# Kernel tuning notes

Hardware: AMD Instinct MI355X
Metric: run time of the kernel (lower is better)

## Reference

```python
import jax, jax.numpy as jnp
import numpy as np

B, C, D, L, H = 128, 1000, 300, 40, 100


def setup_inputs() -> dict:
    key = jax.random.key(0)
    ks = jax.random.split(key, 16)
    def rn(i, shape, sc=1.0):
        return (jax.random.normal(ks[i], shape, jnp.float32) * sc).astype(jnp.float32)
    return {
        "utt": rn(0, (B, L, D)),
        "sys_slots": rn(1, (B, D), 0.1),
        "conf_slots": rn(2, (B, D), 0.1),
        "conf_values": rn(3, (B, D), 0.1),
        "y_past_state": jax.random.uniform(ks[4], (B, C), jnp.float32),
        "slot_emb": rn(5, (C, D), 0.1),
        "value_emb": rn(6, (C, D), 0.1),
        "Wc": rn(7, (D, 2 * D), 0.05), "bc": jnp.zeros((D,), jnp.float32),
        "conv_w1": rn(8, (D, D, 1), 0.05), "conv_b1": jnp.zeros((D,), jnp.float32),
        "conv_w2": rn(9, (D, D, 2), 0.05), "conv_b2": jnp.zeros((D,), jnp.float32),
        "conv_w3": rn(10, (D, D, 3), 0.05), "conv_b3": jnp.zeros((D,), jnp.float32),
        "Wd": rn(11, (H, D), 0.05), "bd": jnp.zeros((H,), jnp.float32),
        "Wmr": rn(12, (H, D), 0.05), "bmr": jnp.zeros((H,), jnp.float32),
        "Wmc": rn(13, (H, D), 0.05), "bmc": jnp.zeros((H,), jnp.float32),
        "Wj": rn(14, (1, H), 0.05), "bj": jnp.zeros((1,), jnp.float32),
    }


def _conv_relu_pool(x_ncl, w, b):
    # x_ncl: [B, D, L]; w: [F, D, k] -> relu(conv) then global max-pool over time -> [B, F]
    y = jax.lax.conv_general_dilated(x_ncl, w, (1,), 'VALID',
                                     dimension_numbers=('NCH', 'OIH', 'NCH'))
    y = jax.nn.relu(y + b[None, :, None])
    return jnp.max(y, axis=2)


def _sig_linear(x, W, b):
    # Sequential(Sigmoid, Linear): Linear applied to sigmoid(x)
    return jax.nn.sigmoid(x) @ W.T + b


def reference(utt, sys_slots, conf_slots, conf_values, y_past_state,
              slot_emb, value_emb, Wc, bc,
              conv_w1, conv_b1, conv_w2, conv_b2, conv_w3, conv_b3,
              Wd, bd, Wmr, bmr, Wmc, bmc, Wj, bj):
    # CNN utterance encoder: sum of 3 conv branches (filter widths 1,2,3)
    x = jnp.transpose(utt, (0, 2, 1))  # [B, D, L]
    final_utt = (_conv_relu_pool(x, conv_w1, conv_b1)
                 + _conv_relu_pool(x, conv_w2, conv_b2)
                 + _conv_relu_pool(x, conv_w3, conv_b3))  # [B, D]

    # candidates_transform = sigmoid(Linear(cat(slot_emb, value_emb)))
    cand = jax.nn.sigmoid(jnp.concatenate([slot_emb, value_emb], axis=1) @ Wc.T + bc)  # [C, D]

    # fused version of the per-batch repeat/addcmul loop: [B, C, D]
    contrib = cand[None, :, :] * final_utt[:, None, :]

    y1 = _sig_linear(_sig_linear(contrib, Wd, bd), Wj, bj)  # [B, C, 1]

    # system-act request gate: ([C,D]@[D,B]) @ [B,D] -> [C, D]
    m_r = (slot_emb @ sys_slots.T) @ final_utt
    y2 = _sig_linear(_sig_linear(m_r, Wmr, bmr), Wj, bj)  # [C, 1]

    # system-act confirm gate
    m_c = ((slot_emb @ conf_slots.T) * (value_emb @ conf_values.T)) @ final_utt  # [C, D]
    y3 = _sig_linear(_sig_linear(m_c, Wmc, bmc), Wj, bj)  # [C, 1]

    y_presoftmax = y1 + y2[None, :, :] + y3[None, :, :]  # [B, C, 1]
    combine = 0.5
    return combine * y_presoftmax[..., 0] + (1.0 - combine) * y_past_state  # [B, C]
```

## Files before the change

kernel.cpp:

```cpp
#include <hip/hip_runtime.h>
#include <hip/hip_bf16.h>

#define OFF_Y23     0
#define OFF_BDP     4096
#define OFF_WJP     4544
#define OFF_BCP     4992
#define OFF_BMRP    6272
#define OFF_BMCP    6720
#define OFF_WALLT   7168
#define OFF_PBF     1235968
#define OFF_FUBF    20896768
#define OFF_FUBFT   20978688
#define OFF_CATSV   21060608
#define OFF_WCPK    22371328
#define OFF_CANDBF  22780928
#define OFF_WDFRAG  23436288
#define OFF_WMRFRAG 23507968
#define OFF_WMCFRAG 23579648
#define OFF_SYSB    23651328
#define OFF_CONFSB  23733248
#define OFF_CONFVB  23815168
#define OFF_PRBF    23897088
#define OFF_PCBF    24159232
#define OFF_SMRBF   24421376
#define OFF_SMCBF   25076736
#define OFF_XBF     25732096

typedef short bf16x8_t __attribute__((ext_vector_type(8)));
typedef float f32x4_t  __attribute__((ext_vector_type(4)));

__device__ __forceinline__ float sigmoidf_fast(float x) {
    return __builtin_amdgcn_rcpf(1.0f + __expf(-x));
}
__device__ __forceinline__ unsigned short f2bf(float x) {
    unsigned int u = __float_as_uint(x);
    unsigned int r = (u + 0x7FFFu + ((u >> 16) & 1u)) >> 16;
    return (unsigned short)r;
}
__device__ __forceinline__ float bf2f(unsigned short h) {
    return __uint_as_float(((unsigned int)h) << 16);
}

__device__ __forceinline__ float frag_fetch(const float* __restrict__ W, int i) {
    int entry = i >> 3, e = i & 7;
    int kt = entry / 448;
    int r = entry - kt * 448;
    int ni = r >> 6, lane = r & 63;
    int j = ni * 16 + (lane & 15);
    int k = kt * 32 + (lane >> 4) * 8 + e;
    return (j < 100 && k < 300) ? W[j * 300 + k] : 0.0f;
}

__global__ void pack_kernel(const float* __restrict__ w1, const float* __restrict__ w2,
                            const float* __restrict__ w3, const float* __restrict__ Wc,
                            const float* __restrict__ Wd, const float* __restrict__ Wmr,
                            const float* __restrict__ Wmc, const float* __restrict__ sys,
                            const float* __restrict__ confs, const float* __restrict__ confv,
                            const float* __restrict__ bd, const float* __restrict__ Wj,
                            const float* __restrict__ bmr, const float* __restrict__ bmc,
                            const float* __restrict__ bc, const float* __restrict__ slot,
                            const float* __restrict__ value, const float* __restrict__ utt,
                            unsigned short* __restrict__ WallTbf,
                            unsigned short* __restrict__ WdFrag,
                            unsigned short* __restrict__ WmrFrag,
                            unsigned short* __restrict__ WmcFrag,
                            float* __restrict__ bdPad, float* __restrict__ WjPad,
                            float* __restrict__ bmrPad, float* __restrict__ bmcPad,
                            float* __restrict__ bcPad,
                            unsigned short* __restrict__ sysB,
                            unsigned short* __restrict__ confsB,
                            unsigned short* __restrict__ confvB,
                            unsigned short* __restrict__ catsv,
                            unsigned short* __restrict__ WcPk,
                            unsigned short* __restrict__ Xbf) {
    int idx = blockIdx.x * blockDim.x + threadIdx.x;
    if (idx < 614400) {
        int tap = idx / 102400;
        int rem = idx - tap * 102400;
        int f = rem / 320, k = rem % 320;
        float v = 0.0f;
        if (f < 300 && k < 300) {
            int fd = f * 300 + k;
            if (tap == 0)      v = w1[fd];
            else if (tap == 1) v = w2[fd * 2 + 0];
            else if (tap == 2) v = w2[fd * 2 + 1];
            else               v = w3[fd * 3 + (tap - 3)];
        }
        WallTbf[idx] = f2bf(v);
    } else if (idx < 650240) {
        int i = idx - 614400;
        WdFrag[i] = f2bf(frag_fetch(Wd, i));
    } else if (idx < 686080) {
        int i = idx - 650240;
        WmrFrag[i] = f2bf(frag_fetch(Wmr, i));
    } else if (idx < 721920) {
        int i = idx - 686080;
        WmcFrag[i] = f2bf(frag_fetch(Wmc, i));
    } else if (idx < 722032) {
        int j = idx - 721920; bdPad[j] = (j < 100) ? bd[j] : 0.0f;
    } else if (idx < 722144) {
        int j = idx - 722032; WjPad[j] = (j < 100) ? Wj[j] : 0.0f;
    } else if (idx < 722256) {
        int j = idx - 722144; bmrPad[j] = (j < 100) ? bmr[j] : 0.0f;
    } else if (idx < 722368) {
        int j = idx - 722256; bmcPad[j] = (j < 100) ? bmc[j] : 0.0f;
    } else if (idx < 722688) {
        int j = idx - 722368; bcPad[j] = (j < 300) ? bc[j] : 0.0f;
    } else if (idx < 845568) {
        int i = idx - 722688;
        int m = i / 40960, r = i % 40960;
        int b = r / 320, k = r % 320;
        const float* src = (m == 0) ? sys : ((m == 1) ? confs : confv);
        unsigned short* dst = (m == 0) ? sysB : ((m == 1) ? confsB : confvB);
        dst[r] = f2bf((k < 300) ? src[b * 300 + k] : 0.0f);
    } else if (idx < 1500928) {
        int i = idx - 845568;
        int c = i / 640, k = i % 640;
        float v = 0.0f;
        if (c < 1000) {
            if (k < 300)                   v = slot[c * 300 + k];
            else if (k >= 320 && k < 620)  v = value[c * 300 + (k - 320)];
        }
        catsv[i] = f2bf(v);
    } else if (idx < 1705728) {
        int i = idx - 1500928;
        int f = i / 640, k = i % 640;
        float v = 0.0f;
        if (f < 300) {
            if (k < 300)                   v = Wc[f * 600 + k];
            else if (k >= 320 && k < 620)  v = Wc[f * 600 + 300 + (k - 320)];
        }
        WcPk[i] = f2bf(v);
    } else if (idx < 3344128) {
        int i = idx - 1705728;
        int m = i / 320, k = i % 320;
        Xbf[i] = f2bf((k < 300) ? utt[m * 300 + k] : 0.0f);
    }
}

__global__ __launch_bounds__(256, 4) void early_kernel(
        const unsigned short* __restrict__ Xbf, const unsigned short* __restrict__ WallTbf,
        unsigned short* __restrict__ Pbf,
        const unsigned short* __restrict__ catsv, const unsigned short* __restrict__ WcPk,
        const float* __restrict__ bcPad, unsigned short* __restrict__ candbf,
        const unsigned short* __restrict__ sysB, const unsigned short* __restrict__ confsB,
        const unsigned short* __restrict__ confvB,
        unsigned short* __restrict__ Prbf, unsigned short* __restrict__ Pcbf) {
    __shared__ __attribute__((aligned(16))) char smem[25600];
    const int bid = blockIdx.x;
    const int tid = threadIdx.x;
    const int lane = tid & 63, w = tid >> 6;
    const int ln = lane & 15, lq = lane >> 4;

    if (bid >= 112) {
        short* As = (short*)smem;
        short* Bs = (short*)(smem + 5120);
        const int g = bid - 112;
        const int xcd = g & 7;
        const int idx2 = g >> 3;
        const int m0 = (xcd * 10 + idx2 / 15) * 64;
        const int n0 = (idx2 % 15) * 128;
        const int arow = tid >> 2, aq = tid & 3;
        f32x4_t acc[4][2];
        #pragma unroll
        for (int i = 0; i < 4; i++)
            #pragma unroll
            for (int j = 0; j < 2; j++) acc[i][j] = (f32x4_t){0.f, 0.f, 0.f, 0.f};

        const unsigned short* aSrc  = Xbf + (m0 + arow) * 320 + aq * 8;
        const unsigned short* bSrc0 = WallTbf + (n0 + arow) * 320 + aq * 8;
        const unsigned short* bSrc1 = WallTbf + (n0 + 64 + arow) * 320 + aq * 8;
        uint4 pa  = *(const uint4*)(aSrc);
        uint4 pb0 = *(const uint4*)(bSrc0);
        uint4 pb1 = *(const uint4*)(bSrc1);
        *(uint4*)(&As[arow * 40 + aq * 8]) = pa;
        *(uint4*)(&Bs[arow * 40 + aq * 8]) = pb0;
        *(uint4*)(&Bs[(64 + arow) * 40 + aq * 8]) = pb1;
        __syncthreads();

        #pragma unroll 1
        for (int kt = 0; kt < 10; kt++) {
            if (kt < 9) {
                int kk2 = (kt + 1) * 32;
                pa  = *(const uint4*)(aSrc + kk2);
                pb0 = *(const uint4*)(bSrc0 + kk2);
                pb1 = *(const uint4*)(bSrc1 + kk2);
            }
            bf16x8_t a[4], b[2];
            #pragma unroll
            for (int mi = 0; mi < 4; mi++)
                a[mi] = *(const bf16x8_t*)(&As[(mi * 16 + ln) * 40 + lq * 8]);
            #pragma unroll
            for (int ni = 0; ni < 2; ni++)
                b[ni] = *(const bf16x8_t*)(&Bs[(w * 32 + ni * 16 + ln) * 40 + lq * 8]);
            #pragma unroll
            for (int mi = 0; mi < 4; mi++)
                #pragma unroll
                for (int ni = 0; ni < 2; ni++)
                    acc[mi][ni] = __builtin_amdgcn_mfma_f32_16x16x32_bf16(a[mi], b[ni], acc[mi][ni], 0, 0, 0);
            if (kt < 9) {
                __syncthreads();
                *(uint4*)(&As[arow * 40 + aq * 8]) = pa;
                *(uint4*)(&Bs[arow * 40 + aq * 8]) = pb0;
                *(uint4*)(&Bs[(64 + arow) * 40 + aq * 8]) = pb1;
                __syncthreads();
            }
        }
        #pragma unroll
        for (int mi = 0; mi < 4; mi++) {
            #pragma unroll
            for (int ni = 0; ni < 2; ni++) {
                int col = n0 + w * 32 + ni * 16 + ln;
                #pragma unroll
                for (int reg = 0; reg < 4; reg++) {
                    int row = m0 + mi * 16 + lq * 4 + reg;
                    Pbf[row * 1920 + col] = f2bf(acc[mi][ni][reg]);
                }
            }
        }
    } else if (bid < 80) {
        short* As = (short*)smem;
        short* Bs = (short*)(smem + 5120);
        const int m0 = (bid / 5) * 64, n0 = (bid % 5) * 64;
        const int wr = w & 1, wc = w >> 1;
        f32x4_t acc[2][2];
        #pragma unroll
        for (int i = 0; i < 2; i++)
            #pragma unroll
            for (int j = 0; j < 2; j++) acc[i][j] = (f32x4_t){0.f, 0.f, 0.f, 0.f};
        const int srow = tid >> 2, sq = tid & 3;
        for (int kk = 0; kk < 640; kk += 32) {
            *(uint4*)(&As[srow * 40 + sq * 8]) = *(const uint4*)(catsv + (m0 + srow) * 640 + kk + sq * 8);
            *(uint4*)(&Bs[srow * 40 + sq * 8]) = *(const uint4*)(WcPk  + (n0 + srow) * 640 + kk + sq * 8);
            __syncthreads();
            bf16x8_t a[2], b[2];
            #pragma unroll
            for (int mi = 0; mi < 2; mi++)
                a[mi] = *(const bf16x8_t*)(&As[(wr * 32 + mi * 16 + ln) * 40 + lq * 8]);
            #pragma unroll
            for (int ni = 0; ni < 2; ni++)
                b[ni] = *(const bf16x8_t*)(&Bs[(wc * 32 + ni * 16 + ln) * 40 + lq * 8]);
            #pragma unroll
            for (int mi = 0; mi < 2; mi++)
                #pragma unroll
                for (int ni = 0; ni < 2; ni++)
                    acc[mi][ni] = __builtin_amdgcn_mfma_f32_16x16x32_bf16(a[mi], b[ni], acc[mi][ni], 0, 0, 0);
            __syncthreads();
        }
        #pragma unroll
        for (int mi = 0; mi < 2; mi++) {
            #pragma unroll
            for (int ni = 0; ni < 2; ni++) {
                int n = n0 + wc * 32 + ni * 16 + ln;
                float bcv = bcPad[n];
                #pragma unroll
                for (int reg = 0; reg < 4; reg++) {
                    int cr = m0 + wr * 32 + mi * 16 + lq * 4 + reg;
                    candbf[cr * 320 + n] = f2bf(sigmoidf_fast(acc[mi][ni][reg] + bcv));
                }
            }
        }
    } else {
        short* As0 = (short*)smem;
        short* As1 = (short*)(smem + 5120);
        short* Bs0 = (short*)(smem + 10240);
        short* Bs1 = (short*)(smem + 15360);
        short* Bs2 = (short*)(smem + 20480);
        const int pid = bid - 80;
        const int c0 = (pid >> 1) * 64;
        const int bh = (pid & 1) * 64;
        f32x4_t accR[4], accS[4], accV[4];
        #pragma unroll
        for (int i = 0; i < 4; i++) {
            accR[i] = (f32x4_t){0.f, 0.f, 0.f, 0.f};
            accS[i] = (f32x4_t){0.f, 0.f, 0.f, 0.f};
            accV[i] = (f32x4_t){0.f, 0.f, 0.f, 0.f};
        }
        for (int kk = 0; kk < 320; kk += 32) {
            #pragma unroll
            for (int i = tid; i < 512; i += 256) {
                int mat = i >> 8, r2 = i & 255;
                int row = r2 >> 2, q = r2 & 3;
                short* dst = mat ? As1 : As0;
                *(uint4*)(&dst[row * 40 + q * 8]) =
                    *(const uint4*)(catsv + (c0 + row) * 640 + mat * 320 + kk + q * 8);
            }
            #pragma unroll
            for (int i = tid; i < 768; i += 256) {
                int mat = i >> 8, r2 = i & 255;
                int row = r2 >> 2, q = r2 & 3;
                const unsigned short* src = (mat == 0) ? sysB : ((mat == 1) ? confsB : confvB);
                short* dst = (mat == 0) ? Bs0 : ((mat == 1) ? Bs1 : Bs2);
                *(uint4*)(&dst[row * 40 + q * 8]) =
                    *(const uint4*)(src + (bh + row) * 320 + kk + q * 8);
            }
            __syncthreads();
            bf16x8_t aS = *(const bf16x8_t*)(&As0[(w * 16 + ln) * 40 + lq * 8]);
            bf16x8_t aV = *(const bf16x8_t*)(&As1[(w * 16 + ln) * 40 + lq * 8]);
            #pragma unroll
            for (int ni = 0; ni < 4; ni++) {
                bf16x8_t bR = *(const bf16x8_t*)(&Bs0[(ni * 16 + ln) * 40 + lq * 8]);
                bf16x8_t bS = *(const bf16x8_t*)(&Bs1[(ni * 16 + ln) * 40 + lq * 8]);
                bf16x8_t bV = *(const bf16x8_t*)(&Bs2[(ni * 16 + ln) * 40 + lq * 8]);
                accR[ni] = __builtin_amdgcn_mfma_f32_16x16x32_bf16(aS, bR, accR[ni], 0, 0, 0);
                accS[ni] = __builtin_amdgcn_mfma_f32_16x16x32_bf16(aS, bS, accS[ni], 0, 0, 0);
                accV[ni] = __builtin_amdgcn_mfma_f32_16x16x32_bf16(aV, bV, accV[ni], 0, 0, 0);
            }
            __syncthreads();
        }
        #pragma unroll
        for (int ni = 0; ni < 4; ni++) {
            int b = bh + ni * 16 + ln;
            #pragma unroll
            for (int reg = 0; reg < 4; reg++) {
                int c = c0 + w * 16 + lq * 4 + reg;
                Prbf[c * 128 + b] = f2bf(accR[ni][reg]);
                Pcbf[c * 128 + b] = f2bf(accS[ni][reg] * accV[ni][reg]);
            }
        }
    }
}

__global__ __launch_bounds__(64) void combine_kernel(const unsigned short* __restrict__ Pbf,
        const float* __restrict__ b1, const float* __restrict__ b2,
        const float* __restrict__ b3, unsigned short* __restrict__ fubf,
        unsigned short* __restrict__ fubfT) {
    int b = blockIdx.x;
    int f = blockIdx.y * 64 + threadIdx.x;
    if (f >= 300) { fubf[b * 320 + f] = 0; fubfT[f * 128 + b] = 0; return; }
    const unsigned short* base = Pbf + (size_t)b * 40 * 1920;
    float m1 = -1e30f, m2 = -1e30f, m3 = -1e30f;
    float p1prev = 0.f, p3prev = 0.f, p3prev2 = 0.f, p4prev = 0.f;
    for (int t = 0; t < 40; ++t) {
        const unsigned short* r = base + t * 1920;
        float p0 = bf2f(r[f]);
        float p1 = bf2f(r[320 + f]);
        float p2 = bf2f(r[640 + f]);
        float p3 = bf2f(r[960 + f]);
        float p4 = bf2f(r[1280 + f]);
        float p5 = bf2f(r[1600 + f]);
        m1 = fmaxf(m1, p0);
        if (t >= 1) m2 = fmaxf(m2, p1prev + p2);
        if (t >= 2) m3 = fmaxf(m3, p3prev2 + p4prev + p5);
        p3prev2 = p3prev; p3prev = p3; p4prev = p4; p1prev = p1;
    }
    float r = fmaxf(m1 + b1[f], 0.f) + fmaxf(m2 + b2[f], 0.f) + fmaxf(m3 + b3[f], 0.f);
    unsigned short rb = f2bf(r);
    fubf[b * 320 + f]  = rb;
    fubfT[f * 128 + b] = rb;
}

__global__ __launch_bounds__(256) void mgate_gemm(const unsigned short* __restrict__ Prbf,
        const unsigned short* __restrict__ Pcbf, const unsigned short* __restrict__ fubfT,
        unsigned short* __restrict__ smrbf, unsigned short* __restrict__ smcbf) {
    __shared__ __attribute__((aligned(16))) short As[2][64 * 40];
    __shared__ __attribute__((aligned(16))) short Bs[64 * 40];
    const int tid = threadIdx.x;
    const int m0 = blockIdx.x * 64, n0 = blockIdx.y * 64;
    const int lane = tid & 63, w = tid >> 6;
    const int wr = w & 1, wc = w >> 1;
    const int ln = lane & 15, lq = lane >> 4;
    f32x4_t accR[2][2], accC[2][2];
    #pragma unroll
    for (int i = 0; i < 2; i++)
        #pragma unroll
        for (int j = 0; j < 2; j++) {
            accR[i][j] = (f32x4_t){0.f, 0.f, 0.f, 0.f};
            accC[i][j] = (f32x4_t){0.f, 0.f, 0.f, 0.f};
        }
    for (int kk = 0; kk < 128; kk += 32) {
        #pragma unroll
        for (int i = tid; i < 512; i += 256) {
            int mat = i >> 8, r2 = i & 255;
            int row = r2 >> 2, q = r2 & 3;
            const unsigned short* src = mat ? Pcbf : Prbf;
            *(uint4*)(&As[mat][row * 40 + q * 8]) =
                *(const uint4*)(src + (m0 + row) * 128 + kk + q * 8);
        }
        if (tid < 256) {
            int row = tid >> 2, q = tid & 3;
            *(uint4*)(&Bs[row * 40 + q * 8]) =
                *(const uint4*)(fubfT + (n0 + row) * 128 + kk + q * 8);
        }
        __syncthreads();
        bf16x8_t aR[2], aC[2], b[2];
        #pragma unroll
        for (int mi = 0; mi < 2; mi++) {
            aR[mi] = *(const bf16x8_t*)(&As[0][(wr * 32 + mi * 16 + ln) * 40 + lq * 8]);
            aC[mi] = *(const bf16x8_t*)(&As[1][(wr * 32 + mi * 16 + ln) * 40 + lq * 8]);
        }
        #pragma unroll
        for (int ni = 0; ni < 2; ni++)
            b[ni] = *(const bf16x8_t*)(&Bs[(wc * 32 + ni * 16 + ln) * 40 + lq * 8]);
        #pragma unroll
        for (int mi = 0; mi < 2; mi++)
            #pragma unroll
            for (int ni = 0; ni < 2; ni++) {
                accR[mi][ni] = __builtin_amdgcn_mfma_f32_16x16x32_bf16(aR[mi], b[ni], accR[mi][ni], 0, 0, 0);
                accC[mi][ni] = __builtin_amdgcn_mfma_f32_16x16x32_bf16(aC[mi], b[ni], accC[mi][ni], 0, 0, 0);
            }
        __syncthreads();
    }
    #pragma unroll
    for (int mi = 0; mi < 2; mi++) {
        #pragma unroll
        for (int ni = 0; ni < 2; ni++) {
            int f = n0 + wc * 32 + ni * 16 + ln;
            #pragma unroll
            for (int reg = 0; reg < 4; reg++) {
                int c = m0 + wr * 32 + mi * 16 + lq * 4 + reg;
                smrbf[c * 320 + f] = f2bf(sigmoidf_fast(accR[mi][ni][reg]));
                smcbf[c * 320 + f] = f2bf(sigmoidf_fast(accC[mi][ni][reg]));
            }
        }
    }
}

__global__ __launch_bounds__(256) void ygate_gemm(const unsigned short* __restrict__ smrbf,
        const unsigned short* __restrict__ smcbf, const unsigned short* __restrict__ WmrFrag,
        const unsigned short* __restrict__ WmcFrag, const float* __restrict__ bmrPad,
        const float* __restrict__ bmcPad, const float* __restrict__ WjPad,
        const float* __restrict__ bj, float* __restrict__ y23) {
    __shared__ __attribute__((aligned(16))) short As[2][64 * 40];
    __shared__ __attribute__((aligned(16))) short Bs[2][3584];
    const int tid = threadIdx.x;
    const int c0 = blockIdx.x * 64;
    const int lane = tid & 63, w = tid >> 6;
    const int ln = lane & 15, lq = lane >> 4;
    f32x4_t accR[7], accC[7];
    #pragma unroll
    for (int i = 0; i < 7; i++) {
        accR[i] = (f32x4_t){0.f, 0.f, 0.f, 0.f};
        accC[i] = (f32x4_t){0.f, 0.f, 0.f, 0.f};
    }
    for (int kt = 0; kt < 10; kt++) {
        int kk = kt * 32;
        #pragma unroll
        for (int i = tid; i < 512; i += 256) {
            int mat = i >> 8, r2 = i & 255;
            int row = r2 >> 2, q = r2 & 3;
            const unsigned short* src = mat ? smcbf : smrbf;
            *(uint4*)(&As[mat][row * 40 + q * 8]) =
                *(const uint4*)(src + (c0 + row) * 320 + kk + q * 8);
        }
        #pragma unroll
        for (int i = tid; i < 896; i += 256) {
            int mat = i / 448, j = i - mat * 448;
            const uint4* s = (const uint4*)((mat ? WmcFrag : WmrFrag) + kt * 3584);
            ((uint4*)&Bs[mat][0])[j] = s[j];
        }
        __syncthreads();
        bf16x8_t aR = *(const bf16x8_t*)(&As[0][(w * 16 + ln) * 40 + lq * 8]);
        bf16x8_t aC = *(const bf16x8_t*)(&As[1][(w * 16 + ln) * 40 + lq * 8]);
        #pragma unroll
        for (int ni = 0; ni < 7; ni++) {
            bf16x8_t bR = *(const bf16x8_t*)(&Bs[0][(ni * 64 + lane) * 8]);
            bf16x8_t bC = *(const bf16x8_t*)(&Bs[1][(ni * 64 + lane) * 8]);
            accR[ni] = __builtin_amdgcn_mfma_f32_16x16x32_bf16(aR, bR, accR[ni], 0, 0, 0);
            accC[ni] = __builtin_amdgcn_mfma_f32_16x16x32_bf16(aC, bC, accC[ni], 0, 0, 0);
        }
        __syncthreads();
    }
    float psum[4] = {0.f, 0.f, 0.f, 0.f};
    #pragma unroll
    for (int ni = 0; ni < 7; ni++) {
        int n = ni * 16 + ln;
        float wj = WjPad[n], br = bmrPad[n], bcv = bmcPad[n];
        #pragma unroll
        for (int reg = 0; reg < 4; reg++) {
            float hr = sigmoidf_fast(accR[ni][reg] + br);
            float hc = sigmoidf_fast(accC[ni][reg] + bcv);
            psum[reg] += (hr + hc) * wj;
        }
    }
    #pragma unroll
    for (int reg = 0; reg < 4; reg++) {
        float v = psum[reg];
        v += __shfl_xor(v, 1);
        v += __shfl_xor(v, 2);
        v += __shfl_xor(v, 4);
        v += __shfl_xor(v, 8);
        if (ln == 0) {
            int c = c0 + w * 16 + lq * 4 + reg;
            y23[c] = v + 2.0f * bj[0];
        }
    }
}

__global__ __launch_bounds__(256) void gemm2_kernel(const unsigned short* __restrict__ candbf,
        const unsigned short* __restrict__ fubf, const unsigned short* __restrict__ WdFrag,
        const float* __restrict__ bdPad, const float* __restrict__ WjPad,
        const float* __restrict__ bj, const float* __restrict__ y23,
        const float* __restrict__ ypast, float* __restrict__ out) {
    __shared__ __attribute__((aligned(16))) short Bs[2][3584];
    __shared__ float bdS[112], WjS[112], ybuf[128];
    const int c = blockIdx.x;
    const int tid = threadIdx.x;
    const int lane = tid & 63, w = tid >> 6;
    const int ln = lane & 15, lq = lane >> 4;
    if (tid < 112) { bdS[tid] = bdPad[tid]; WjS[tid] = WjPad[tid]; }

    const unsigned short* candRow = candbf + c * 320;
    const unsigned short* fuR0 = fubf + (w * 32 + ln) * 320;
    const unsigned short* fuR1 = fuR0 + 16 * 320;

    f32x4_t acc[2][7];
    #pragma unroll
    for (int mi = 0; mi < 2; mi++)
        #pragma unroll
        for (int ni = 0; ni < 7; ni++) acc[mi][ni] = (f32x4_t){0.f, 0.f, 0.f, 0.f};

    {
        const uint4* src = (const uint4*)(WdFrag);
        uint4* dst = (uint4*)&Bs[0][0];
        dst[tid] = src[tid];
        if (tid < 192) dst[tid + 256] = src[tid + 256];
    }
    __syncthreads();

    #pragma unroll
    for (int kt = 0; kt < 10; kt++) {
        if (kt < 9) {
            const uint4* src = (const uint4*)(WdFrag + (kt + 1) * 3584);
            uint4* dst = (uint4*)&Bs[(kt + 1) & 1][0];
            dst[tid] = src[tid];
            if (tid < 192) dst[tid + 256] = src[tid + 256];
        }
        const int k0 = kt * 32 + lq * 8;
        bf16x8_t cf  = *(const bf16x8_t*)(candRow + k0);
        bf16x8_t f0v = *(const bf16x8_t*)(fuR0 + k0);
        bf16x8_t f1v = *(const bf16x8_t*)(fuR1 + k0);
        bf16x8_t a0, a1;
        #pragma unroll
        for (int e = 0; e < 8; e += 2) {
            float cv0 = bf2f((unsigned short)cf[e]);
            float cv1 = bf2f((unsigned short)cf[e + 1]);
            float2 s0 = make_float2(sigmoidf_fast(cv0 * bf2f((unsigned short)f0v[e])),
                                    sigmoidf_fast(cv1 * bf2f((unsigned short)f0v[e + 1])));
            float2 s1 = make_float2(sigmoidf_fast(cv0 * bf2f((unsigned short)f1v[e])),
                                    sigmoidf_fast(cv1 * bf2f((unsigned short)f1v[e + 1])));
            __hip_bfloat162 p0 = __float22bfloat162_rn(s0);
            __hip_bfloat162 p1 = __float22bfloat162_rn(s1);
            ((unsigned int*)&a0)[e >> 1] = *(unsigned int*)&p0;
            ((unsigned int*)&a1)[e >> 1] = *(unsigned int*)&p1;
        }
        #pragma unroll
        for (int ni = 0; ni < 7; ni++) {
            bf16x8_t bfr = *(const bf16x8_t*)(&Bs[kt & 1][(ni * 64 + lane) * 8]);
            acc[0][ni] = __builtin_amdgcn_mfma_f32_16x16x32_bf16(a0, bfr, acc[0][ni], 0, 0, 0);
            acc[1][ni] = __builtin_amdgcn_mfma_f32_16x16x32_bf16(a1, bfr, acc[1][ni], 0, 0, 0);
        }
        __syncthreads();
    }

    float psum[2][4] = {{0.f, 0.f, 0.f, 0.f}, {0.f, 0.f, 0.f, 0.f}};
    #pragma unroll
    for (int mi = 0; mi < 2; mi++) {
        #pragma unroll
        for (int ni = 0; ni < 7; ni++) {
            int n = ni * 16 + ln;
            float bdv = bdS[n], wjv = WjS[n];
            #pragma unroll
            for (int reg = 0; reg < 4; reg++) {
                float h = sigmoidf_fast(acc[mi][ni][reg] + bdv);
                psum[mi][reg] += h * wjv;
            }
        }
    }
    #pragma unroll
    for (int mi = 0; mi < 2; mi++) {
        #pragma unroll
        for (int reg = 0; reg < 4; reg++) {
            float v = psum[mi][reg];
            v += __shfl_xor(v, 1);
            v += __shfl_xor(v, 2);
            v += __shfl_xor(v, 4);
            v += __shfl_xor(v, 8);
            if (ln == 0) ybuf[w * 32 + mi * 16 + lq * 4 + reg] = v;
        }
    }
    __syncthreads();
    if (tid < 128) {
        int b = tid;
        float y1 = ybuf[b] + bj[0];
        out[b * 1000 + c] = 0.5f * (y1 + y23[c]) + 0.5f * ypast[b * 1000 + c];
    }
}

extern "C" void kernel_launch(void* const* d_in, const int* in_sizes, int n_in,
                              void* d_out, int out_size, void* d_ws, size_t ws_size,
                              hipStream_t stream) {
    const float* utt   = (const float*)d_in[0];
    const float* sys   = (const float*)d_in[1];
    const float* confs = (const float*)d_in[2];
    const float* confv = (const float*)d_in[3];
    const float* ypast = (const float*)d_in[4];
    const float* slot  = (const float*)d_in[5];
    const float* value = (const float*)d_in[6];
    const float* Wc    = (const float*)d_in[7];
    const float* bc    = (const float*)d_in[8];
    const float* w1    = (const float*)d_in[9];
    const float* b1    = (const float*)d_in[10];
    const float* w2    = (const float*)d_in[11];
    const float* b2    = (const float*)d_in[12];
    const float* w3    = (const float*)d_in[13];
    const float* b3    = (const float*)d_in[14];
    const float* Wd    = (const float*)d_in[15];
    const float* bd    = (const float*)d_in[16];
    const float* Wmr   = (const float*)d_in[17];
    const float* bmr   = (const float*)d_in[18];
    const float* Wmc   = (const float*)d_in[19];
    const float* bmc   = (const float*)d_in[20];
    const float* Wj    = (const float*)d_in[21];
    const float* bj    = (const float*)d_in[22];

    char* wsb = (char*)d_ws;
    float* y23    = (float*)(wsb + OFF_Y23);
    float* bdPad  = (float*)(wsb + OFF_BDP);
    float* WjPad  = (float*)(wsb + OFF_WJP);
    float* bcPad  = (float*)(wsb + OFF_BCP);
    float* bmrPad = (float*)(wsb + OFF_BMRP);
    float* bmcPad = (float*)(wsb + OFF_BMCP);
    unsigned short* WallTbf = (unsigned short*)(wsb + OFF_WALLT);
    unsigned short* Pbf     = (unsigned short*)(wsb + OFF_PBF);
    unsigned short* fubf    = (unsigned short*)(wsb + OFF_FUBF);
    unsigned short* fubfT   = (unsigned short*)(wsb + OFF_FUBFT);
    unsigned short* catsv   = (unsigned short*)(wsb + OFF_CATSV);
    unsigned short* WcPk    = (unsigned short*)(wsb + OFF_WCPK);
    unsigned short* candbf  = (unsigned short*)(wsb + OFF_CANDBF);
    unsigned short* WdFrag  = (unsigned short*)(wsb + OFF_WDFRAG);
    unsigned short* WmrFrag = (unsigned short*)(wsb + OFF_WMRFRAG);
    unsigned short* WmcFrag = (unsigned short*)(wsb + OFF_WMCFRAG);
    unsigned short* sysB    = (unsigned short*)(wsb + OFF_SYSB);
    unsigned short* confsB  = (unsigned short*)(wsb + OFF_CONFSB);
    unsigned short* confvB  = (unsigned short*)(wsb + OFF_CONFVB);
    unsigned short* Prbf    = (unsigned short*)(wsb + OFF_PRBF);
    unsigned short* Pcbf    = (unsigned short*)(wsb + OFF_PCBF);
    unsigned short* smrbf   = (unsigned short*)(wsb + OFF_SMRBF);
    unsigned short* smcbf   = (unsigned short*)(wsb + OFF_SMCBF);
    unsigned short* Xbf     = (unsigned short*)(wsb + OFF_XBF);
    float* out = (float*)d_out;

    pack_kernel<<<13063, 256, 0, stream>>>(w1, w2, w3, Wc, Wd, Wmr, Wmc, sys, confs, confv,
                                           bd, Wj, bmr, bmc, bc, slot, value, utt,
                                           WallTbf, WdFrag, WmrFrag, WmcFrag,
                                           bdPad, WjPad, bmrPad, bmcPad, bcPad,
                                           sysB, confsB, confvB, catsv, WcPk, Xbf);
    early_kernel<<<1312, 256, 0, stream>>>(Xbf, WallTbf, Pbf,
                                           catsv, WcPk, bcPad, candbf,
                                           sysB, confsB, confvB, Prbf, Pcbf);
    combine_kernel<<<dim3(128, 5), 64, 0, stream>>>(Pbf, b1, b2, b3, fubf, fubfT);
    mgate_gemm<<<dim3(16, 5), 256, 0, stream>>>(Prbf, Pcbf, fubfT, smrbf, smcbf);
    ygate_gemm<<<16, 256, 0, stream>>>(smrbf, smcbf, WmrFrag, WmcFrag,
                                       bmrPad, bmcPad, WjPad, bj, y23);
    gemm2_kernel<<<1000, 256, 0, stream>>>(candbf, fubf, WdFrag, bdPad, WjPad,
                                           bj, y23, ypast, out);
}
```

Before: 192.6 us.

## Fuse conv max-pool combine into conv GEMM and vectorize pack kernel

The conv GEMM is retiled so that each block computes one batch element's 40 time steps for 32 filters across all six taps. The shift-add, max-pool, bias and ReLU are then done from shared memory inside the same block. This removes the large intermediate Pbf buffer (about 20 MB of bf16 traffic) and the separate combine kernel launch. Separately, the pack kernel now converts 8 elements per thread and writes them with 16-byte stores. In exchange, the GEMM tiles are smaller (48x192, with part of the A rows padded) and a single warp does the serial pooling epilogue, which could lower MFMA efficiency in that phase.

Result: slower. 214.5 us (+11.4%).

```diff
diff --git a/kernel.cpp b/kernel.cpp
--- a/kernel.cpp
+++ b/kernel.cpp
@@ -8,23 +8,22 @@
 #define OFF_BMRP    6272
 #define OFF_BMCP    6720
 #define OFF_WALLT   7168
-#define OFF_PBF     1235968
-#define OFF_FUBF    20896768
-#define OFF_FUBFT   20978688
-#define OFF_CATSV   21060608
-#define OFF_WCPK    22371328
-#define OFF_CANDBF  22780928
-#define OFF_WDFRAG  23436288
-#define OFF_WMRFRAG 23507968
-#define OFF_WMCFRAG 23579648
-#define OFF_SYSB    23651328
-#define OFF_CONFSB  23733248
-#define OFF_CONFVB  23815168
-#define OFF_PRBF    23897088
-#define OFF_PCBF    24159232
-#define OFF_SMRBF   24421376
-#define OFF_SMCBF   25076736
-#define OFF_XBF     25732096
+#define OFF_FUBF    1235968
+#define OFF_FUBFT   1317888
+#define OFF_CATSV   1399808
+#define OFF_WCPK    2710528
+#define OFF_CANDBF  3120128
+#define OFF_WDFRAG  3775488
+#define OFF_WMRFRAG 3847168
+#define OFF_WMCFRAG 3918848
+#define OFF_SYSB    3990528
+#define OFF_CONFSB  4072448
+#define OFF_CONFVB  4154368
+#define OFF_PRBF    4236288
+#define OFF_PCBF    4498432
+#define OFF_SMRBF   4760576
+#define OFF_SMCBF   5415936
+#define OFF_XBF     6071296
 
 typedef short bf16x8_t __attribute__((ext_vector_type(8)));
 typedef float f32x4_t  __attribute__((ext_vector_type(4)));
@@ -41,106 +40,131 @@
     return __uint_as_float(((unsigned int)h) << 16);
 }
 
-__device__ __forceinline__ float frag_fetch(const float* __restrict__ W, int i) {
-    int entry = i >> 3, e = i & 7;
-    int kt = entry / 448;
-    int r = entry - kt * 448;
-    int ni = r >> 6, lane = r & 63;
-    int j = ni * 16 + (lane & 15);
-    int k = kt * 32 + (lane >> 4) * 8 + e;
-    return (j < 100 && k < 300) ? W[j * 300 + k] : 0.0f;
-}
-
-__global__ void pack_kernel(const float* __restrict__ w1, const float* __restrict__ w2,
-                            const float* __restrict__ w3, const float* __restrict__ Wc,
-                            const float* __restrict__ Wd, const float* __restrict__ Wmr,
-                            const float* __restrict__ Wmc, const float* __restrict__ sys,
-                            const float* __restrict__ confs, const float* __restrict__ confv,
-                            const float* __restrict__ bd, const float* __restrict__ Wj,
-                            const float* __restrict__ bmr, const float* __restrict__ bmc,
-                            const float* __restrict__ bc, const float* __restrict__ slot,
-                            const float* __restrict__ value, const float* __restrict__ utt,
-                            unsigned short* __restrict__ WallTbf,
-                            unsigned short* __restrict__ WdFrag,
-                            unsigned short* __restrict__ WmrFrag,
-                            unsigned short* __restrict__ WmcFrag,
-                            float* __restrict__ bdPad, float* __restrict__ WjPad,
-                            float* __restrict__ bmrPad, float* __restrict__ bmcPad,
-                            float* __restrict__ bcPad,
-                            unsigned short* __restrict__ sysB,
-                            unsigned short* __restrict__ confsB,
-                            unsigned short* __restrict__ confvB,
-                            unsigned short* __restrict__ catsv,
-                            unsigned short* __restrict__ WcPk,
-                            unsigned short* __restrict__ Xbf) {
-    int idx = blockIdx.x * blockDim.x + threadIdx.x;
-    if (idx < 614400) {
-        int tap = idx / 102400;
-        int rem = idx - tap * 102400;
-        int f = rem / 320, k = rem % 320;
-        float v = 0.0f;
-        if (f < 300 && k < 300) {
-            int fd = f * 300 + k;
-            if (tap == 0)      v = w1[fd];
-            else if (tap == 1) v = w2[fd * 2 + 0];
-            else if (tap == 2) v = w2[fd * 2 + 1];
-            else               v = w3[fd * 3 + (tap - 3)];
-        }
-        WallTbf[idx] = f2bf(v);
-    } else if (idx < 650240) {
-        int i = idx - 614400;
-        WdFrag[i] = f2bf(frag_fetch(Wd, i));
-    } else if (idx < 686080) {
-        int i = idx - 650240;
-        WmrFrag[i] = f2bf(frag_fetch(Wmr, i));
-    } else if (idx < 721920) {
-        int i = idx - 686080;
-        WmcFrag[i] = f2bf(frag_fetch(Wmc, i));
-    } else if (idx < 722032) {
-        int j = idx - 721920; bdPad[j] = (j < 100) ? bd[j] : 0.0f;
-    } else if (idx < 722144) {
-        int j = idx - 722032; WjPad[j] = (j < 100) ? Wj[j] : 0.0f;
-    } else if (idx < 722256) {
-        int j = idx - 722144; bmrPad[j] = (j < 100) ? bmr[j] : 0.0f;
-    } else if (idx < 722368) {
-        int j = idx - 722256; bmcPad[j] = (j < 100) ? bmc[j] : 0.0f;
-    } else if (idx < 722688) {
-        int j = idx - 722368; bcPad[j] = (j < 300) ? bc[j] : 0.0f;
-    } else if (idx < 845568) {
-        int i = idx - 722688;
-        int m = i / 40960, r = i % 40960;
-        int b = r / 320, k = r % 320;
+__global__ __launch_bounds__(256) void pack_kernel(const float* __restrict__ w1,
+        const float* __restrict__ w2, const float* __restrict__ w3,
+        const float* __restrict__ Wc, const float* __restrict__ Wd,
+        const float* __restrict__ Wmr, const float* __restrict__ Wmc,
+        const float* __restrict__ sys, const float* __restrict__ confs,
+        const float* __restrict__ confv, const float* __restrict__ bd,
+        const float* __restrict__ Wj, const float* __restrict__ bmr,
+        const float* __restrict__ bmc, const float* __restrict__ bc,
+        const float* __restrict__ slot, const float* __restrict__ value,
+        const float* __restrict__ utt,
+        unsigned short* __restrict__ WallTbf, unsigned short* __restrict__ WdFrag,
+        unsigned short* __restrict__ WmrFrag, unsigned short* __restrict__ WmcFrag,
+        float* __restrict__ bdPad, float* __restrict__ WjPad,
+        float* __restrict__ bmrPad, float* __restrict__ bmcPad,
+        float* __restrict__ bcPad,
+        unsigned short* __restrict__ sysB, unsigned short* __restrict__ confsB,
+        unsigned short* __restrict__ confvB, unsigned short* __restrict__ catsv,
+        unsigned short* __restrict__ WcPk, unsigned short* __restrict__ Xbf) {
+    int t = blockIdx.x * 256 + threadIdx.x;
+    union { unsigned short u[8]; uint4 q; } o;
+    if (t < 76800) {
+        int i8 = t * 8;
+        int tap = i8 / 102400;
+        int rem = i8 - tap * 102400;
+        int f = rem / 320, k0 = rem % 320;
+        #pragma unroll
+        for (int e = 0; e < 8; e++) {
+            int k = k0 + e;
+            float v = 0.0f;
+            if (f < 300 && k < 300) {
+                int fd = f * 300 + k;
+                v = (tap == 0) ? w1[fd] : (tap == 1) ? w2[fd * 2]
+                  : (tap == 2) ? w2[fd * 2 + 1] : w3[fd * 3 + (tap - 3)];
+            }
+            o.u[e] = f2bf(v);
+        }
+        *(uint4*)(WallTbf + i8) = o.q;
+    } else if (t < 90240) {
+        int ent = t - 76800;
+        int mat = ent / 4480;
+        int le = ent - mat * 4480;
+        const float* W = (mat == 0) ? Wd : ((mat == 1) ? Wmr : Wmc);
+        unsigned short* dst = (mat == 0) ? WdFrag : ((mat == 1) ? WmrFrag : WmcFrag);
+        int kt = le / 448;
+        int r = le - kt * 448;
+        int ni = r >> 6, lane = r & 63;
+        int j = ni * 16 + (lane & 15);
+        int kb = kt * 32 + (lane >> 4) * 8;
+        #pragma unroll
+        for (int e = 0; e < 8; e++) {
+            int k = kb + e;
+            o.u[e] = f2bf((j < 100 && k < 300) ? W[j * 300 + k] : 0.0f);
+        }
+        *(uint4*)(dst + le * 8) = o.q;
+    } else if (t < 105600) {
+        int i8 = (t - 90240) * 8;
+        int m = i8 / 40960, r = i8 - m * 40960;
+        int bb = r / 320, k0 = r % 320;
         const float* src = (m == 0) ? sys : ((m == 1) ? confs : confv);
         unsigned short* dst = (m == 0) ? sysB : ((m == 1) ? confsB : confvB);
-        dst[r] = f2bf((k < 300) ? src[b * 300 + k] : 0.0f);
-    } else if (idx < 1500928) {
-        int i = idx - 845568;
-        int c = i / 640, k = i % 640;
-        float v = 0.0f;
-        if (c < 1000) {
-            if (k < 300)                   v = slot[c * 300 + k];
-            else if (k >= 320 && k < 620)  v = value[c * 300 + (k - 320)];
-        }
-        catsv[i] = f2bf(v);
-    } else if (idx < 1705728) {
-        int i = idx - 1500928;
-        int f = i / 640, k = i % 640;
-        float v = 0.0f;
-        if (f < 300) {
-            if (k < 300)                   v = Wc[f * 600 + k];
-            else if (k >= 320 && k < 620)  v = Wc[f * 600 + 300 + (k - 320)];
-        }
-        WcPk[i] = f2bf(v);
-    } else if (idx < 3344128) {
-        int i = idx - 1705728;
-        int m = i / 320, k = i % 320;
-        Xbf[i] = f2bf((k < 300) ? utt[m * 300 + k] : 0.0f);
+        #pragma unroll
+        for (int e = 0; e < 8; e++) {
+            int k = k0 + e;
+            o.u[e] = f2bf((k < 300) ? src[bb * 300 + k] : 0.0f);
+        }
+        *(uint4*)(dst + r) = o.q;
+    } else if (t < 187520) {
+        int i8 = (t - 105600) * 8;
+        int c = i8 / 640, k0 = i8 % 640;
+        #pragma unroll
+        for (int e = 0; e < 8; e++) {
+            int k = k0 + e;
+            float v = 0.0f;
+            if (c < 1000) {
+                if (k < 300)                  v = slot[c * 300 + k];
+                else if (k >= 320 && k < 620) v = value[c * 300 + (k - 320)];
+            }
+            o.u[e] = f2bf(v);
+        }
+        *(uint4*)(catsv + i8) = o.q;
+    } else if (t < 213120) {
+        int i8 = (t - 187520) * 8;
+        int f = i8 / 640, k0 = i8 % 640;
+        #pragma unroll
+        for (int e = 0; e < 8; e++) {
+            int k = k0 + e;
+            float v = 0.0f;
+            if (f < 300) {
+                if (k < 300)                  v = Wc[f * 600 + k];
+                else if (k >= 320 && k < 620) v = Wc[f * 600 + 300 + (k - 320)];
+            }
+            o.u[e] = f2bf(v);
+        }
+        *(uint4*)(WcPk + i8) = o.q;
+    } else if (t < 417920) {
+        int i8 = (t - 213120) * 8;
+        int m = i8 / 320, k0 = i8 % 320;
+        if (k0 + 8 <= 300) {
+            float4 a = *(const float4*)(utt + m * 300 + k0);
+            float4 b = *(const float4*)(utt + m * 300 + k0 + 4);
+            o.u[0] = f2bf(a.x); o.u[1] = f2bf(a.y); o.u[2] = f2bf(a.z); o.u[3] = f2bf(a.w);
+            o.u[4] = f2bf(b.x); o.u[5] = f2bf(b.y); o.u[6] = f2bf(b.z); o.u[7] = f2bf(b.w);
+        } else {
+            #pragma unroll
+            for (int e = 0; e < 8; e++) {
+                int k = k0 + e;
+                o.u[e] = f2bf((k < 300) ? utt[m * 300 + k] : 0.0f);
+            }
+        }
+        *(uint4*)(Xbf + i8) = o.q;
+    } else if (t < 418688) {
+        int j = t - 417920;
+        if (j < 112)      bdPad[j] = (j < 100) ? bd[j] : 0.0f;
+        else if (j < 224) { int jj = j - 112; WjPad[jj]  = (jj < 100) ? Wj[jj]  : 0.0f; }
+        else if (j < 336) { int jj = j - 224; bmrPad[jj] = (jj < 100) ? bmr[jj] : 0.0f; }
+        else if (j < 448) { int jj = j - 336; bmcPad[jj] = (jj < 100) ? bmc[jj] : 0.0f; }
+        else              { int jj = j - 448; bcPad[jj]  = (jj < 300) ? bc[jj]  : 0.0f; }
     }
 }
 
 __global__ __launch_bounds__(256, 4) void early_kernel(
         const unsigned short* __restrict__ Xbf, const unsigned short* __restrict__ WallTbf,
-        unsigned short* __restrict__ Pbf,
+        const float* __restrict__ b1, const float* __restrict__ b2,
+        const float* __restrict__ b3,
+        unsigned short* __restrict__ fubf, unsigned short* __restrict__ fubfT,
         const unsigned short* __restrict__ catsv, const unsigned short* __restrict__ WcPk,
         const float* __restrict__ bcPad, unsigned short* __restrict__ candbf,
         const unsigned short* __restrict__ sysB, const unsigned short* __restrict__ confsB,
@@ -154,68 +178,111 @@
 
     if (bid >= 112) {
         short* As = (short*)smem;
-        short* Bs = (short*)(smem + 5120);
+        short* Bs = (short*)(smem + 3840);
+        short* Ps = (short*)smem;
         const int g = bid - 112;
         const int xcd = g & 7;
         const int idx2 = g >> 3;
-        const int m0 = (xcd * 10 + idx2 / 15) * 64;
-        const int n0 = (idx2 % 15) * 128;
+        const int b = xcd * 16 + idx2 / 10;
+        const int fb = idx2 % 10;
+        f32x4_t acc[3][3];
+        #pragma unroll
+        for (int i = 0; i < 3; i++)
+            #pragma unroll
+            for (int j = 0; j < 3; j++) acc[i][j] = (f32x4_t){0.f, 0.f, 0.f, 0.f};
+
         const int arow = tid >> 2, aq = tid & 3;
-        f32x4_t acc[4][2];
-        #pragma unroll
-        for (int i = 0; i < 4; i++)
-            #pragma unroll
-            for (int j = 0; j < 2; j++) acc[i][j] = (f32x4_t){0.f, 0.f, 0.f, 0.f};
-
-        const unsigned short* aSrc  = Xbf + (m0 + arow) * 320 + aq * 8;
-        const unsigned short* bSrc0 = WallTbf + (n0 + arow) * 320 + aq * 8;
-        const unsigned short* bSrc1 = WallTbf + (n0 + 64 + arow) * 320 + aq * 8;
-        uint4 pa  = *(const uint4*)(aSrc);
-        uint4 pb0 = *(const uint4*)(bSrc0);
-        uint4 pb1 = *(const uint4*)(bSrc1);
-        *(uint4*)(&As[arow * 40 + aq * 8]) = pa;
-        *(uint4*)(&Bs[arow * 40 + aq * 8]) = pb0;
-        *(uint4*)(&Bs[(64 + arow) * 40 + aq * 8]) = pb1;
+        int agrow = b * 40 + arow; if (agrow > 5119) agrow = 5119;
+        const unsigned short* aSrc = Xbf + agrow * 320 + aq * 8;
+        const unsigned short* bSrc[3];
+        #pragma unroll
+        for (int s = 0; s < 3; s++) {
+            int i2 = tid + 256 * s;
+            int nr = i2 >> 2, q = i2 & 3;
+            int tap = nr >> 5, f = fb * 32 + (nr & 31);
+            bSrc[s] = WallTbf + (tap * 320 + f) * 320 + q * 8;
+        }
+        uint4 pa = {0, 0, 0, 0}, pb[3];
+        if (tid < 192) pa = *(const uint4*)aSrc;
+        #pragma unroll
+        for (int s = 0; s < 3; s++) pb[s] = *(const uint4*)bSrc[s];
+        if (tid < 192) *(uint4*)(&As[arow * 40 + aq * 8]) = pa;
+        #pragma unroll
+        for (int s = 0; s < 3; s++) {
+            int i2 = tid + 256 * s;
+            int nr = i2 >> 2, q = i2 & 3;
+            *(uint4*)(&Bs[nr * 40 + q * 8]) = pb[s];
+        }
         __syncthreads();
 
         #pragma unroll 1
         for (int kt = 0; kt < 10; kt++) {
             if (kt < 9) {
                 int kk2 = (kt + 1) * 32;
-                pa  = *(const uint4*)(aSrc + kk2);
-                pb0 = *(const uint4*)(bSrc0 + kk2);
-                pb1 = *(const uint4*)(bSrc1 + kk2);
-            }
-            bf16x8_t a[4], b[2];
-            #pragma unroll
-            for (int mi = 0; mi < 4; mi++)
+                if (tid < 192) pa = *(const uint4*)(aSrc + kk2);
+                #pragma unroll
+                for (int s = 0; s < 3; s++) pb[s] = *(const uint4*)(bSrc[s] + kk2);
+            }
+            bf16x8_t a[3], bb[3];
+            #pragma unroll
+            for (int mi = 0; mi < 3; mi++)
                 a[mi] = *(const bf16x8_t*)(&As[(mi * 16 + ln) * 40 + lq * 8]);
             #pragma unroll
-            for (int ni = 0; ni < 2; ni++)
-                b[ni] = *(const bf16x8_t*)(&Bs[(w * 32 + ni * 16 + ln) * 40 + lq * 8]);
-            #pragma unroll
-            for (int mi = 0; mi < 4; mi++)
+            for (int ni = 0; ni < 3; ni++)
+                bb[ni] = *(const bf16x8_t*)(&Bs[(w * 48 + ni * 16 + ln) * 40 + lq * 8]);
+            #pragma unroll
+            for (int mi = 0; mi < 3; mi++)
                 #pragma unroll
-                for (int ni = 0; ni < 2; ni++)
-                    acc[mi][ni] = __builtin_amdgcn_mfma_f32_16x16x32_bf16(a[mi], b[ni], acc[mi][ni], 0, 0, 0);
+                for (int ni = 0; ni < 3; ni++)
+                    acc[mi][ni] = __builtin_amdgcn_mfma_f32_16x16x32_bf16(a[mi], bb[ni], acc[mi][ni], 0, 0, 0);
             if (kt < 9) {
                 __syncthreads();
-                *(uint4*)(&As[arow * 40 + aq * 8]) = pa;
-                *(uint4*)(&Bs[arow * 40 + aq * 8]) = pb0;
-                *(uint4*)(&Bs[(64 + arow) * 40 + aq * 8]) = pb1;
+                if (tid < 192) *(uint4*)(&As[arow * 40 + aq * 8]) = pa;
+                #pragma unroll
+                for (int s = 0; s < 3; s++) {
+                    int i2 = tid + 256 * s;
+                    int nr = i2 >> 2, q = i2 & 3;
+                    *(uint4*)(&Bs[nr * 40 + q * 8]) = pb[s];
+                }
                 __syncthreads();
             }
         }
-        #pragma unroll
-        for (int mi = 0; mi < 4; mi++) {
-            #pragma unroll
-            for (int ni = 0; ni < 2; ni++) {
-                int col = n0 + w * 32 + ni * 16 + ln;
+        __syncthreads();
+        #pragma unroll
+        for (int mi = 0; mi < 3; mi++)
+            #pragma unroll
+            for (int ni = 0; ni < 3; ni++)
                 #pragma unroll
-                for (int reg = 0; reg < 4; reg++) {
-                    int row = m0 + mi * 16 + lq * 4 + reg;
-                    Pbf[row * 1920 + col] = f2bf(acc[mi][ni][reg]);
+                for (int reg = 0; reg < 4; reg++)
+                    Ps[(mi * 16 + lq * 4 + reg) * 200 + (w * 48 + ni * 16 + ln)] =
+                        (short)f2bf(acc[mi][ni][reg]);
+        __syncthreads();
+        if (tid < 32) {
+            int f = fb * 32 + tid;
+            if (f < 300) {
+                float m1 = -1e30f, m2 = -1e30f, m3 = -1e30f;
+                float p1prev = 0.f, p3prev = 0.f, p3prev2 = 0.f, p4prev = 0.f;
+                for (int tt = 0; tt < 40; ++tt) {
+                    const short* r = Ps + tt * 200;
+                    float p0 = bf2f((unsigned short)r[tid]);
+                    float p1 = bf2f((unsigned short)r[32 + tid]);
+                    float p2 = bf2f((unsigned short)r[64 + tid]);
+                    float p3 = bf2f((unsigned short)r[96 + tid]);
+                    float p4 = bf2f((unsigned short)r[128 + tid]);
+                    float p5 = bf2f((unsigned short)r[160 + tid]);
+                    m1 = fmaxf(m1, p0);
+                    if (tt >= 1) m2 = fmaxf(m2, p1prev + p2);
+                    if (tt >= 2) m3 = fmaxf(m3, p3prev2 + p4prev + p5);
+                    p3prev2 = p3prev; p3prev = p3; p4prev = p4; p1prev = p1;
                 }
+                float r = fmaxf(m1 + b1[f], 0.f) + fmaxf(m2 + b2[f], 0.f)
+                        + fmaxf(m3 + b3[f], 0.f);
+                unsigned short rb = f2bf(r);
+                fubf[b * 320 + f]  = rb;
+                fubfT[f * 128 + b] = rb;
+            } else {
+                fubf[b * 320 + f]  = 0;
+                fubfT[f * 128 + b] = 0;
             }
         }
     } else if (bid < 80) {
@@ -319,35 +386,6 @@
             }
         }
     }
-}
-
-__global__ __launch_bounds__(64) void combine_kernel(const unsigned short* __restrict__ Pbf,
-        const float* __restrict__ b1, const float* __restrict__ b2,
-        const float* __restrict__ b3, unsigned short* __restrict__ fubf,
-        unsigned short* __restrict__ fubfT) {
-    int b = blockIdx.x;
-    int f = blockIdx.y * 64 + threadIdx.x;
-    if (f >= 300) { fubf[b * 320 + f] = 0; fubfT[f * 128 + b] = 0; return; }
-    const unsigned short* base = Pbf + (size_t)b * 40 * 1920;
-    float m1 = -1e30f, m2 = -1e30f, m3 = -1e30f;
-    float p1prev = 0.f, p3prev = 0.f, p3prev2 = 0.f, p4prev = 0.f;
-    for (int t = 0; t < 40; ++t) {
-        const unsigned short* r = base + t * 1920;
-        float p0 = bf2f(r[f]);
-        float p1 = bf2f(r[320 + f]);
-        float p2 = bf2f(r[640 + f]);
-        float p3 = bf2f(r[960 + f]);
-        float p4 = bf2f(r[1280 + f]);
-        float p5 = bf2f(r[1600 + f]);
-        m1 = fmaxf(m1, p0);
-        if (t >= 1) m2 = fmaxf(m2, p1prev + p2);
-        if (t >= 2) m3 = fmaxf(m3, p3prev2 + p4prev + p5);
-        p3prev2 = p3prev; p3prev = p3; p4prev = p4; p1prev = p1;
-    }
-    float r = fmaxf(m1 + b1[f], 0.f) + fmaxf(m2 + b2[f], 0.f) + fmaxf(m3 + b3[f], 0.f);
-    unsigned short rb = f2bf(r);
-    fubf[b * 320 + f]  = rb;
-    fubfT[f * 128 + b] = rb;
 }
 
 __global__ __launch_bounds__(256) void mgate_gemm(const unsigned short* __restrict__ Prbf,
@@ -622,7 +660,6 @@
     float* bmrPad = (float*)(wsb + OFF_BMRP);
     float* bmcPad = (float*)(wsb + OFF_BMCP);
     unsigned short* WallTbf = (unsigned short*)(wsb + OFF_WALLT);
-    unsigned short* Pbf     = (unsigned short*)(wsb + OFF_PBF);
     unsigned short* fubf    = (unsigned short*)(wsb + OFF_FUBF);
     unsigned short* fubfT   = (unsigned short*)(wsb + OFF_FUBFT);
     unsigned short* catsv   = (unsigned short*)(wsb + OFF_CATSV);
@@ -641,15 +678,14 @@
     unsigned short* Xbf     = (unsigned short*)(wsb + OFF_XBF);
     float* out = (float*)d_out;
 
-    pack_kernel<<<13063, 256, 0, stream>>>(w1, w2, w3, Wc, Wd, Wmr, Wmc, sys, confs, confv,
-                                           bd, Wj, bmr, bmc, bc, slot, value, utt,
-                                           WallTbf, WdFrag, WmrFrag, WmcFrag,
-                                           bdPad, WjPad, bmrPad, bmcPad, bcPad,
-                                           sysB, confsB, confvB, catsv, WcPk, Xbf);
-    early_kernel<<<1312, 256, 0, stream>>>(Xbf, WallTbf, Pbf,
+    pack_kernel<<<1636, 256, 0, stream>>>(w1, w2, w3, Wc, Wd, Wmr, Wmc, sys, confs, confv,
+                                          bd, Wj, bmr, bmc, bc, slot, value, utt,
+                                          WallTbf, WdFrag, WmrFrag, WmcFrag,
+                                          bdPad, WjPad, bmrPad, bmcPad, bcPad,
+                                          sysB, confsB, confvB, catsv, WcPk, Xbf);
+    early_kernel<<<1392, 256, 0, stream>>>(Xbf, WallTbf, b1, b2, b3, fubf, fubfT,
                                            catsv, WcPk, bcPad, candbf,
                                            sysB, confsB, confvB, Prbf, Pcbf);
-    combine_kernel<<<dim3(128, 5), 64, 0, stream>>>(Pbf, b1, b2, b3, fubf, fubfT);
     mgate_gemm<<<dim3(16, 5), 256, 0, stream>>>(Prbf, Pcbf, fubfT, smrbf, smcbf);
     ygate_gemm<<<16, 256, 0, stream>>>(smrbf, smcbf, WmrFrag, WmcFrag,
                                        bmrPad, bmcPad, WjPad, bj, y23);
```
